# Kernel tuning notes

Hardware: AMD Instinct MI355X
Metric: run time of the kernel (lower is better)

Reference implementation:

```python
import jax, jax.numpy as jnp
import numpy as np

B, N, L = 16, 128, 512            # batch, scan length, per-step feature (= configs.seq_len)
D, S, K, R, H = 1024, 16, 4, 64, 2048  # d_model, d_state, ker_size, dt_rank, hidden_dimention


def _mamba_params(key, scale=0.02):
    ks = jax.random.split(key, 6)
    return dict(
        in_w=jax.random.normal(ks[0], (2 * D, L)) * scale,
        conv_w=jax.random.normal(ks[1], (D, K)) * scale,
        conv_b=jnp.zeros((D,)),
        xproj_w=jax.random.normal(ks[2], (R + 2 * S, D)) * scale,
        dt_w=jax.random.normal(ks[3], (D, R)) * scale,
        dt_b=jax.random.normal(ks[4], (D,)) * scale,
        A_log=jnp.tile(jnp.log(jnp.arange(1, S + 1, dtype=jnp.float32)), (D, 1)),
        Dp=jnp.ones((D,)),
        out_w=jax.random.normal(ks[5], (L, D)) * scale,
    )


def setup_inputs():
    key = jax.random.key(0)
    kx, kf, kr, k1, k2 = jax.random.split(key, 5)
    inp = {"x": jax.random.normal(kx, (B, N, L), dtype=jnp.float32)}
    for pre, k in (("f_", kf), ("r_", kr)):
        for n, v in _mamba_params(k).items():
            inp[pre + n] = v
    inp["pu_w"] = jax.random.normal(k1, (H, L)) * 0.02
    inp["pu_b"] = jnp.zeros((H,))
    inp["pl_w"] = jax.random.normal(k2, (L, H)) * 0.02
    inp["pl_b"] = jnp.zeros((L,))
    inp["ln_g"] = jnp.ones((L,))
    inp["ln_b"] = jnp.zeros((L,))
    return inp


def _ln(x, g, b, eps=1e-5):
    m = x.mean(-1, keepdims=True)
    v = ((x - m) ** 2).mean(-1, keepdims=True)
    return (x - m) * jax.lax.rsqrt(v + eps) * g + b


def _dw_causal_conv(x, w, b):
    # x: [B,N,D]; depthwise causal conv along N with kernel [D,K]
    xt = jnp.pad(x.transpose(0, 2, 1), ((0, 0), (0, 0), (K - 1, 0)))  # [B,D,N+K-1]
    y = jax.lax.conv_general_dilated(xt, w[:, None, :], (1,), 'VALID',
                                     dimension_numbers=('NCH', 'OIH', 'NCH'),
                                     feature_group_count=D)
    return (y + b[None, :, None]).transpose(0, 2, 1)


def _mamba(x, in_w, conv_w, conv_b, xproj_w, dt_w, dt_b, A_log, Dp, out_w):
    # standard Mamba block (in_proj -> depthwise conv -> silu -> selective scan -> gate -> out_proj)
    xi, res = jnp.split(x @ in_w.T, 2, axis=-1)             # [B,N,D] each
    xc = jax.nn.silu(_dw_causal_conv(xi, conv_w, conv_b))   # [B,N,D]
    dbc = xc @ xproj_w.T                                    # [B,N,R+2S]
    dt, Bm, Cm = dbc[..., :R], dbc[..., R:R + S], dbc[..., R + S:]
    delta = jax.nn.softplus(dt @ dt_w.T + dt_b)             # [B,N,D]
    A = -jnp.exp(A_log)                                     # [D,S]
    dA = jnp.exp(delta[..., None] * A)                      # [B,N,D,S]
    dBx = delta[..., None] * Bm[:, :, None, :] * xc[..., None]

    def step(h, t):
        dA_t, dBx_t, C_t = t
        h = dA_t * h + dBx_t                                # [B,D,S]
        return h, jnp.einsum('bds,bs->bd', h, C_t)

    _, ys = jax.lax.scan(step, jnp.zeros((x.shape[0], D, S), x.dtype),
                         (dA.transpose(1, 0, 2, 3), dBx.transpose(1, 0, 2, 3), Cm.transpose(1, 0, 2)))
    y = ys.transpose(1, 0, 2) + xc * Dp                     # [B,N,D]
    y = y * jax.nn.silu(res)
    return y @ out_w.T                                      # [B,N,L]


def reference(x, f_in_w, f_conv_w, f_conv_b, f_xproj_w, f_dt_w, f_dt_b, f_A_log, f_Dp, f_out_w,
              r_in_w, r_conv_w, r_conv_b, r_xproj_w, r_dt_w, r_dt_b, r_A_log, r_Dp, r_out_w,
              pu_w, pu_b, pl_w, pl_b, ln_g, ln_b):
    y1 = _mamba(x, f_in_w, f_conv_w, f_conv_b, f_xproj_w, f_dt_w, f_dt_b, f_A_log, f_Dp, f_out_w)
    y2 = _mamba(x[:, ::-1, :], r_in_w, r_conv_w, r_conv_b, r_xproj_w, r_dt_w, r_dt_b, r_A_log, r_Dp, r_out_w)
    y3 = _ln(x + y1 + y2[:, ::-1, :], ln_g, ln_b)
    yp = jax.nn.relu(y3 @ pu_w.T + pu_b)
    yp = yp @ pl_w.T + pl_b
    return _ln(yp + y3, ln_g, ln_b)
```

## Files before the change

### kernel.cpp

```cpp
#include <hip/hip_runtime.h>
#include <hip/hip_bf16.h>
#include <cstdint>

typedef __hip_bfloat16 bf16;

constexpr int Bb = 16, Nn = 128, Ll = 512, Dd = 1024, Ss = 16, Rr = 64, Hh = 2048;
constexpr int Mm = Bb * Nn;
#define LOG2E 1.44269504088896340736f

using bf16x8 = __attribute__((ext_vector_type(8))) __bf16;
using bf16x4 = __attribute__((ext_vector_type(4))) __bf16;
using f32x4  = __attribute__((ext_vector_type(4))) float;

__device__ __forceinline__ float to_f(float x) { return x; }
__device__ __forceinline__ float to_f(bf16 x) { return __bfloat162float(x); }
__device__ __forceinline__ void store_t(float* p, float v) { *p = v; }
__device__ __forceinline__ void store_t(bf16* p, float v) { *p = __float2bfloat16(v); }
__device__ __forceinline__ __bf16 cvt1(float x) {
  bf16 h = __float2bfloat16(x);
  return *reinterpret_cast<__bf16*>(&h);
}
__device__ __forceinline__ float bfraw_to_f(__bf16 x) {
  bf16 h = *reinterpret_cast<bf16*>(&x);
  return __bfloat162float(h);
}
__device__ __forceinline__ bf16x8 load8(const bf16* p) { return *(const bf16x8*)p; }
__device__ __forceinline__ bf16x8 load8(const float* p) {
  float4 a = *(const float4*)p;
  float4 b = *(const float4*)(p + 4);
  bf16x8 r;
  r[0] = cvt1(a.x); r[1] = cvt1(a.y); r[2] = cvt1(a.z); r[3] = cvt1(a.w);
  r[4] = cvt1(b.x); r[5] = cvt1(b.y); r[6] = cvt1(b.z); r[7] = cvt1(b.w);
  return r;
}
__device__ __forceinline__ bf16x8 load8rt(const void* p, size_t idx, int isbf) {
  if (isbf) return load8((const bf16*)p + idx);
  return load8((const float*)p + idx);
}
__device__ __forceinline__ float ldf(const void* p, int i, int isbf) {
  if (isbf) return __bfloat162float(((const bf16*)p)[i]);
  return ((const float*)p)[i];
}
__device__ __forceinline__ void gld16(const bf16* g, __bf16* l) {
  __builtin_amdgcn_global_load_lds(
      (const __attribute__((address_space(1))) void*)g,
      (__attribute__((address_space(3))) void*)l, 16, 0, 0);
}

enum { EPI_STORE = 0, EPI_BIAS_RELU = 1, EPI_ADD = 3, EPI_BIAS = 4, EPI_BIAS_SOFTPLUS = 5,
       EPI_ATOMIC = 6 };

__global__ void sniff_kernel(const unsigned short* __restrict__ xs, int* __restrict__ flags) {
  const int tid = threadIdx.x;
  int cnt = 0;
  for (int j = 0; j < 64; ++j) {
    int i = tid + j * 256;
    unsigned short u = xs[(size_t)i * 64];
    bf16 h = *reinterpret_cast<bf16*>(&u);
    float v = __bfloat162float(h);
    float a = fabsf(v);
    if (v == 0.f || (a > 0.0009765625f && a < 16.f)) ++cnt;
  }
  __shared__ int sc[256];
  sc[tid] = cnt;
  __syncthreads();
  for (int o = 128; o > 0; o >>= 1) {
    if (tid < o) sc[tid] += sc[tid + o];
    __syncthreads();
  }
  if (tid == 0) flags[0] = (sc[0] > 8192) ? 1 : 0;
}

__global__ __launch_bounds__(256) void prep_kernel(
    const int* __restrict__ flagp, const void* __restrict__ x,
    float* __restrict__ ZB, unsigned short* __restrict__ Xb,
    float* __restrict__ zerop,
    const void* __restrict__ fin, const void* __restrict__ rin,
    const void* __restrict__ fout, const void* __restrict__ rout,
    const void* __restrict__ puw, const void* __restrict__ plw,
    bf16* __restrict__ WBin, bf16* __restrict__ WBout,
    bf16* __restrict__ WBpu, bf16* __restrict__ WBpl) {
  const int isbf = *flagp;
  const int i = blockIdx.x * 256 + threadIdx.x;
  if (i < 262144) {
    float4 o;
    ushort4 u;
    if (isbf) {
      u = ((const ushort4*)x)[i];
      bf16 h0 = *reinterpret_cast<bf16*>(&u.x), h1 = *reinterpret_cast<bf16*>(&u.y);
      bf16 h2 = *reinterpret_cast<bf16*>(&u.z), h3 = *reinterpret_cast<bf16*>(&u.w);
      o = float4{__bfloat162float(h0), __bfloat162float(h1),
                 __bfloat162float(h2), __bfloat162float(h3)};
    } else {
      o = ((const float4*)x)[i];
      bf16 h0 = __float2bfloat16(o.x), h1 = __float2bfloat16(o.y);
      bf16 h2 = __float2bfloat16(o.z), h3 = __float2bfloat16(o.w);
      u = ushort4{*(unsigned short*)&h0, *(unsigned short*)&h1,
                  *(unsigned short*)&h2, *(unsigned short*)&h3};
    }
    ((float4*)ZB)[i] = o;
    ((ushort4*)Xb)[i] = u;
  } else if (i < 622592) {
    ((float4*)zerop)[i - 262144] = float4{0.f, 0.f, 0.f, 0.f};
  } else {
    const int j = i - 622592;
    const void* src;
    bf16* dst;
    int si;
    if (j < 131072) { src = fin; si = j; dst = WBin + (size_t)si * 8; }
    else if (j < 262144) { src = rin; si = j - 131072; dst = WBin + (size_t)1048576 + (size_t)si * 8; }
    else if (j < 393216) { src = puw; si = j - 262144; dst = WBpu + (size_t)si * 8; }
    else if (j < 524288) { src = plw; si = j - 393216; dst = WBpl + (size_t)si * 8; }
    else if (j < 589824) {
      src = fout; si = j - 524288;
      int e = si * 8;
      dst = WBout + (size_t)(e >> 10) * 2048 + (e & 1023);
    } else {
      src = rout; si = j - 589824;
      int e = si * 8;
      dst = WBout + (size_t)(e >> 10) * 2048 + 1024 + (e & 1023);
    }
    *(bf16x8*)dst = load8rt(src, (size_t)si * 8, isbf);
  }
}

constexpr int LDT2 = 72;

template <typename TC, int EPI>
__global__ __launch_bounds__(256) void gemm_rt(
    const int* __restrict__ flagp,
    const void* __restrict__ A, int lda, int abf,
    const void* __restrict__ Bw, const void* __restrict__ Bw2, int ldb,
    int bmode, int bsplit,
    TC* __restrict__ C, int ldc,
    const void* __restrict__ bias, const void* __restrict__ bias2,
    int N, int Kchunk, int zk, size_t a_doff, size_t c_doff) {
  const int isbf = *flagp;
  const int ab = (abf == 2) ? isbf : abf;
  __shared__ __align__(16) __bf16 As[64 * LDT2];
  __shared__ __align__(16) __bf16 Bs[64 * LDT2];
  const int tid = threadIdx.x;
  const int wave = tid >> 6, lane = tid & 63;
  const int quad = lane >> 4, l16 = lane & 15;
  const int wm = wave & 1, wn = wave >> 1;
  int bx = blockIdx.x, by = blockIdx.y;
  const int gx = gridDim.x, gy = gridDim.y;
  if ((gx & 7) == 0) {
    int id = bx + gx * by;
    int xcd = id & 7, sl = id >> 3;
    by = sl % gy;
    bx = (sl / gy) * 8 + xcd;
  }
  int zsl = blockIdx.z;
  const void* Ap = A;
  const void* Bp0 = Bw;
  const void* biasp = bias;
  if (bmode == 3) {
    const int dir = zsl / zk;
    zsl = zsl % zk;
    if (dir) {
      Ap = (const char*)A + a_doff * (size_t)(ab ? 2 : 4);
      C += c_doff;
      Bp0 = Bw2;
      biasp = bias2;
    }
  }
  const int m0 = by * 64, n0 = bx * 64;
  const int kb = zsl * Kchunk;
  const int srow = tid >> 3;
  const int scol = (tid & 7) * 8;
  f32x4 acc[2][2] = {};
  for (int k0 = kb; k0 < kb + Kchunk; k0 += 64) {
#pragma unroll
    for (int h = 0; h < 2; ++h) {
      int r = srow + h * 32;
      *(bf16x8*)(&As[r * LDT2 + scol]) =
          load8rt(Ap, (size_t)(m0 + r) * lda + k0 + scol, ab);
      int rb = n0 + r;
      rb = rb < N ? rb : N - 1;
      size_t bi = (size_t)rb * ldb + k0 + scol;
      *(bf16x8*)(&Bs[r * LDT2 + scol]) = load8rt(Bp0, bi, isbf);
    }
    __syncthreads();
#pragma unroll
    for (int kk2 = 0; kk2 < 2; ++kk2) {
      bf16x8 af[2], bfr[2];
#pragma unroll
      for (int i = 0; i < 2; ++i)
        af[i] = *(const bf16x8*)(&As[(wm * 32 + i * 16 + l16) * LDT2 + kk2 * 32 + quad * 8]);
#pragma unroll
      for (int j = 0; j < 2; ++j)
        bfr[j] = *(const bf16x8*)(&Bs[(wn * 32 + j * 16 + l16) * LDT2 + kk2 * 32 + quad * 8]);
#pragma unroll
      for (int i = 0; i < 2; ++i)
#pragma unroll
        for (int j = 0; j < 2; ++j)
          acc[i][j] = __builtin_amdgcn_mfma_f32_16x16x32_bf16(af[i], bfr[j], acc[i][j], 0, 0, 0);
    }
    __syncthreads();
  }
#pragma unroll
  for (int i = 0; i < 2; ++i) {
#pragma unroll
    for (int j = 0; j < 2; ++j) {
      const int col = n0 + wn * 32 + j * 16 + l16;
      if (col >= N) continue;
      float bv = 0.f;
      if (EPI == EPI_BIAS_RELU || EPI == EPI_BIAS || EPI == EPI_BIAS_SOFTPLUS)
        bv = ldf(biasp, col, isbf);
#pragma unroll
      for (int r = 0; r < 4; ++r) {
        const int row = m0 + wm * 32 + i * 16 + quad * 4 + r;
        size_t idx = (size_t)row * ldc + col;
        float v = acc[i][j][r];
        if (EPI == EPI_STORE) store_t(&C[idx], v);
        else if (EPI == EPI_BIAS_RELU) { v += bv; store_t(&C[idx], v > 0.f ? v : 0.f); }
        else if (EPI == EPI_BIAS) store_t(&C[idx], v + bv);
        else if (EPI == EPI_BIAS_SOFTPLUS) {
          v += bv;
          store_t(&C[idx], (v > 20.f) ? v : log1pf(__expf(v)));
        } else if (EPI == EPI_ATOMIC) {
          atomicAdd((float*)&C[idx], v);
        }
      }
    }
  }
}

template <typename TC, int EPI>
__global__ __launch_bounds__(256) void gemm128n(
    const int* __restrict__ flagp,
    const bf16* __restrict__ A, int lda,
    const bf16* __restrict__ Bw, int ldb,
    TC* __restrict__ C, int ldc,
    const void* __restrict__ bias,
    int Kchunk) {
  __shared__ __align__(16) __bf16 As[128 * 64];
  __shared__ __align__(16) __bf16 Bs[128 * 64];
  const int tid = threadIdx.x;
  const int wave = tid >> 6, lane = tid & 63;
  const int quad = lane >> 4, l16 = lane & 15;
  const int wr = wave >> 1, wc = wave & 1;
  int bx = blockIdx.x, by = blockIdx.y;
  const int gx = gridDim.x, gy = gridDim.y;
  if ((gx & 7) == 0) {
    int id = bx + gx * by;
    int xcd = id & 7, sl = id >> 3;
    by = sl % gy;
    bx = (sl / gy) * 8 + xcd;
  }
  const int m0 = by * 128, n0 = bx * 128;
  const int kb = blockIdx.z * Kchunk;
  const int lr = lane >> 3;
  const int lc = (lane & 7) * 8;
  f32x4 acc[4][4] = {};
  for (int k0 = kb; k0 < kb + Kchunk; k0 += 64) {
#pragma unroll
    for (int rr = 0; rr < 4; ++rr) {
      const int rowb = rr * 32 + wave * 8;
      gld16(A + (size_t)(m0 + rowb + lr) * lda + k0 + lc, &As[rowb * 64]);
      gld16(Bw + (size_t)(n0 + rowb + lr) * ldb + k0 + lc, &Bs[rowb * 64]);
    }
    __syncthreads();
#pragma unroll
    for (int kk = 0; kk < 2; ++kk) {
      bf16x8 af[4], bfr[4];
#pragma unroll
      for (int i = 0; i < 4; ++i)
        af[i] = *(const bf16x8*)(&As[(wr * 64 + i * 16 + l16) * 64 + kk * 32 + quad * 8]);
#pragma unroll
      for (int j = 0; j < 4; ++j)
        bfr[j] = *(const bf16x8*)(&Bs[(wc * 64 + j * 16 + l16) * 64 + kk * 32 + quad * 8]);
#pragma unroll
      for (int i = 0; i < 4; ++i)
#pragma unroll
        for (int j = 0; j < 4; ++j)
          acc[i][j] = __builtin_amdgcn_mfma_f32_16x16x32_bf16(af[i], bfr[j], acc[i][j], 0, 0, 0);
    }
    __syncthreads();
  }
  const int isbf = *flagp;
#pragma unroll
  for (int i = 0; i < 4; ++i) {
#pragma unroll
    for (int j = 0; j < 4; ++j) {
      const int col = n0 + wc * 64 + j * 16 + l16;
      float bv = 0.f;
      if (EPI == EPI_BIAS_RELU) bv = ldf(bias, col, isbf);
#pragma unroll
      for (int r = 0; r < 4; ++r) {
        const int row = m0 + wr * 64 + i * 16 + quad * 4 + r;
        size_t idx = (size_t)row * ldc + col;
        float v = acc[i][j][r];
        if (EPI == EPI_STORE) store_t(&C[idx], v);
        else if (EPI == EPI_BIAS_RELU) { v += bv; store_t(&C[idx], v > 0.f ? v : 0.f); }
        else if (EPI == EPI_ATOMIC) atomicAdd((float*)&C[idx], v);
      }
    }
  }
}

__global__ __launch_bounds__(256) void conv_silu_rt(
    const int* __restrict__ flagp, const bf16* __restrict__ X2b,
    const void* __restrict__ fcw, const void* __restrict__ fcb,
    const void* __restrict__ rcw, const void* __restrict__ rcb,
    bf16* __restrict__ XCb) {
  const int isbf = *flagp;
  const int dir = blockIdx.y >> 2;
  const int d = (blockIdx.y & 3) * 256 + threadIdx.x;
  const int m = blockIdx.x;
  const int t = m & (Nn - 1);
  const void* cw = dir ? rcw : fcw;
  const void* cb = dir ? rcb : fcb;
  float w0 = ldf(cw, d * 4 + 0, isbf), w1 = ldf(cw, d * 4 + 1, isbf);
  float w2 = ldf(cw, d * 4 + 2, isbf), w3 = ldf(cw, d * 4 + 3, isbf);
  float a = ldf(cb, d, isbf);
  const size_t base = (size_t)m * 4096 + (size_t)dir * 2048 + d;
  if (dir == 0) {
    if (t >= 3) a += w0 * to_f(X2b[base - 3 * 4096]);
    if (t >= 2) a += w1 * to_f(X2b[base - 2 * 4096]);
    if (t >= 1) a += w2 * to_f(X2b[base - 1 * 4096]);
    a += w3 * to_f(X2b[base]);
  } else {
    if (t + 3 < Nn) a += w0 * to_f(X2b[base + 3 * 4096]);
    if (t + 2 < Nn) a += w1 * to_f(X2b[base + 2 * 4096]);
    if (t + 1 < Nn) a += w2 * to_f(X2b[base + 1 * 4096]);
    a += w3 * to_f(X2b[base]);
  }
  const float s = a / (1.f + __builtin_amdgcn_exp2f(-a * LOG2E));
  XCb[(size_t)m * 2048 + (size_t)dir * 1024 + d] = __float2bfloat16(s);
}

__global__ __launch_bounds__(128) void scan_gate4(
    const int* __restrict__ flagp,
    const float* __restrict__ DBC0, bf16* __restrict__ XCb, const bf16* __restrict__ X2b,
    const bf16* __restrict__ DELTA0,
    const void* __restrict__ fAlog, const void* __restrict__ fDp,
    const void* __restrict__ rAlog, const void* __restrict__ rDp) {
  const int isbf = *flagp;
  const int dir = blockIdx.z;
  const float* DBC = DBC0 + (size_t)dir * Mm * 96;
  const bf16* DELTA = DELTA0 + (size_t)dir * Mm * 1024;
  const void* A_log = dir ? rAlog : fAlog;
  const void* Dp = dir ? rDp : fDp;
  __shared__ __align__(16) __bf16 sBC[Nn * 32];
  __shared__ __align__(16) __bf16 sD[Nn * 32];
  __shared__ __align__(16) __bf16 sX[Nn * 32];
  __shared__ __align__(16) __bf16 sG[Nn * 32];
  __shared__ __align__(16) __bf16 sY[Nn * 32];
  const int b = blockIdx.x;
  const int d0 = blockIdx.y * 32;
  const int tid = threadIdx.x;
  const size_t rowbase = (size_t)b * Nn;
  const size_t xc_col = (size_t)dir * 1024;
#pragma unroll
  for (int k = 0; k < 8; ++k) {
    int idx = tid + k * 128;
    int t = idx >> 3, c = idx & 7;
    float4 v = *(const float4*)(DBC + (rowbase + t) * 96 + 64 + c * 4);
    bf16x4 pv = {cvt1(v.x), cvt1(v.y), cvt1(v.z), cvt1(v.w)};
    int dst = (c < 4) ? (t * 32 + c * 8) : (t * 32 + (c - 4) * 8 + 4);
    *(bf16x4*)&sBC[dst] = pv;
  }
#pragma unroll
  for (int k = 0; k < 4; ++k) {
    int idx = tid + k * 128;
    int t = idx >> 2, h = idx & 3;
    *(uint4*)&sD[t * 32 + h * 8] =
        *(const uint4*)(DELTA + (rowbase + t) * 1024 + d0 + h * 8);
    *(uint4*)&sX[t * 32 + h * 8] =
        *(const uint4*)(XCb + (rowbase + t) * 2048 + xc_col + d0 + h * 8);
    bf16x8 rv = *(const bf16x8*)(X2b + (rowbase + t) * 4096 + (size_t)dir * 2048 + 1024 + d0 + h * 8);
    bf16x8 gv;
#pragma unroll
    for (int e = 0; e < 8; ++e) {
      float r = bfraw_to_f(rv[e]);
      gv[e] = cvt1(r / (1.f + __builtin_amdgcn_exp2f(-r * LOG2E)));
    }
    *(bf16x8*)&sG[t * 32 + h * 8] = gv;
  }
  __syncthreads();
  const int wv = tid >> 6, lane = tid & 63;
  const int dl = lane & 15, sg = lane >> 4;
  const int d_local = wv * 16 + dl;
  const int d = d0 + d_local;
  float A_[4];
#pragma unroll
  for (int j = 0; j < 4; ++j)
    A_[j] = -__expf(ldf(A_log, d * Ss + sg * 4 + j, isbf)) * LOG2E;
  const float dp = ldf(Dp, d, isbf);
  float h0 = 0.f, h1 = 0.f, h2 = 0.f, h3 = 0.f;
  for (int pg = 0; pg < Nn / 8; ++pg) {
    float accs[8], xvs[8];
#pragma unroll
    for (int u = 0; u < 8; ++u) {
      const int p = pg * 8 + u;
      const int t = dir ? (Nn - 1 - p) : p;
      const float dv = bfraw_to_f(sD[t * 32 + d_local]);
      const float xv = bfraw_to_f(sX[t * 32 + d_local]);
      bf16x8 bc = *(const bf16x8*)&sBC[t * 32 + sg * 8];
      const float dx = dv * xv;
      h0 = __builtin_amdgcn_exp2f(dv * A_[0]) * h0 + dx * bfraw_to_f(bc[0]);
      h1 = __builtin_amdgcn_exp2f(dv * A_[1]) * h1 + dx * bfraw_to_f(bc[1]);
      h2 = __builtin_amdgcn_exp2f(dv * A_[2]) * h2 + dx * bfraw_to_f(bc[2]);
      h3 = __builtin_amdgcn_exp2f(dv * A_[3]) * h3 + dx * bfraw_to_f(bc[3]);
      accs[u] = h0 * bfraw_to_f(bc[4]) + h1 * bfraw_to_f(bc[5]) +
                h2 * bfraw_to_f(bc[6]) + h3 * bfraw_to_f(bc[7]);
      xvs[u] = xv;
    }
#pragma unroll
    for (int u = 0; u < 8; ++u) {
      float a = accs[u];
      a += __shfl_xor(a, 16, 64);
      a += __shfl_xor(a, 32, 64);
      if (sg == 0) {
        const int p = pg * 8 + u;
        const int t = dir ? (Nn - 1 - p) : p;
        const float g = bfraw_to_f(sG[t * 32 + d_local]);
        sY[t * 32 + d_local] = cvt1((a + xvs[u] * dp) * g);
      }
    }
  }
  __syncthreads();
#pragma unroll
  for (int k = 0; k < 4; ++k) {
    int idx = tid + k * 128;
    int t = idx >> 2, h = idx & 3;
    *(uint4*)(XCb + (rowbase + t) * 2048 + xc_col + d0 + h * 8) =
        *(const uint4*)&sY[t * 32 + h * 8];
  }
}

template <int MODE>
__global__ __launch_bounds__(256) void ln_rt(const int* __restrict__ flagp,
                                             const float* __restrict__ Z,
                                             const float* __restrict__ Zadd,
                                             const void* __restrict__ g,
                                             const void* __restrict__ bb,
                                             const void* __restrict__ pb,
                                             void* __restrict__ outp,
                                             bf16* __restrict__ outp2) {
  const int isbf = *flagp;
  const int row = blockIdx.x;
  const int tid = threadIdx.x;
  const int c0 = tid * 2;
  const float2* z = (const float2*)(Z + (size_t)row * Ll);
  float2 v = z[tid];
  if (MODE == 1) {
    const float2* za = (const float2*)(Zadd + (size_t)row * Ll);
    float2 a = za[tid];
    v.x += a.x + ldf(pb, c0, isbf);
    v.y += a.y + ldf(pb, c0 + 1, isbf);
  }
  float s = v.x + v.y, q = v.x * v.x + v.y * v.y;
#pragma unroll
  for (int o = 32; o > 0; o >>= 1) {
    s += __shfl_xor(s, o, 64);
    q += __shfl_xor(q, o, 64);
  }
  __shared__ float ss[4], qq[4];
  const int wv = tid >> 6, ln = tid & 63;
  if (ln == 0) { ss[wv] = s; qq[wv] = q; }
  __syncthreads();
  s = ss[0] + ss[1] + ss[2] + ss[3];
  q = qq[0] + qq[1] + qq[2] + qq[3];
  const float mean = s * (1.f / Ll);
  const float var = q * (1.f / Ll) - mean * mean;
  const float rs = rsqrtf(var + 1e-5f);
  const float o0 = (v.x - mean) * rs * ldf(g, c0, isbf) + ldf(bb, c0, isbf);
  const float o1 = (v.y - mean) * rs * ldf(g, c0 + 1, isbf) + ldf(bb, c0 + 1, isbf);
  if (MODE == 0) {
    float* out = (float*)outp;
    out[(size_t)row * Ll + c0] = o0;
    out[(size_t)row * Ll + c0 + 1] = o1;
    outp2[(size_t)row * Ll + c0] = __float2bfloat16(o0);
    outp2[(size_t)row * Ll + c0 + 1] = __float2bfloat16(o1);
  } else {
    if (isbf) {
      bf16* out = (bf16*)outp;
      out[(size_t)row * Ll + c0] = __float2bfloat16(o0);
      out[(size_t)row * Ll + c0 + 1] = __float2bfloat16(o1);
    } else {
      float* out = (float*)outp;
      out[(size_t)row * Ll + c0] = o0;
      out[(size_t)row * Ll + c0 + 1] = o1;
    }
  }
}

extern "C" void kernel_launch(void* const* d_in, const int* in_sizes, int n_in, void* d_out,
                              int out_size, void* d_ws, size_t ws_size, hipStream_t stream) {
  char* ws = (char*)d_ws;
  int* flags = (int*)ws;
  bf16* X2b = (bf16*)(ws + 256);
  bf16* XCb = X2b + (size_t)Mm * 4096;
  bf16* Y3b = XCb + (size_t)Mm * 2048;
  bf16* DELTA = Y3b + (size_t)Mm * 512;
  bf16* Xb = DELTA + (size_t)2 * Mm * 1024;
  bf16* WBin = Xb + (size_t)Mm * 512;
  bf16* WBout = WBin + (size_t)4096 * 512;
  bf16* WBpu = WBout + (size_t)512 * 2048;
  bf16* WBpl = WBpu + (size_t)2048 * 512;
  float* DBC = (float*)(WBpl + (size_t)512 * 2048);
  float* Z2 = DBC + (size_t)2 * Mm * 96;
  float* ZB = Z2 + (size_t)Mm * 512;
  float* Y3 = ZB + (size_t)Mm * 512;
  bf16* H1 = X2b;
  size_t needed = 256 +
                  2 * ((size_t)Mm * 4096 + (size_t)Mm * 2048 + (size_t)Mm * 512 +
                       (size_t)2 * Mm * 1024 + (size_t)Mm * 512 +
                       (size_t)4096 * 512 + (size_t)512 * 2048 +
                       (size_t)2048 * 512 + (size_t)512 * 2048) +
                  4 * ((size_t)2 * Mm * 96 + (size_t)3 * Mm * 512);
  if (ws_size < needed) return;

  const void* x = d_in[0];
  const dim3 blk(256);

  sniff_kernel<<<dim3(1), blk, 0, stream>>>((const unsigned short*)x, flags);
  prep_kernel<<<dim3(4992), blk, 0, stream>>>(
      flags, x, ZB, (unsigned short*)Xb, DBC,
      d_in[1], d_in[10], d_in[9], d_in[18], d_in[19], d_in[21],
      WBin, WBout, WBpu, WBpl);
  gemm128n<bf16, EPI_STORE><<<dim3(32, 16), blk, 0, stream>>>(
      flags, Xb, Ll, WBin, Ll, X2b, 4096, nullptr, Ll);
  conv_silu_rt<<<dim3(Mm, 8), blk, 0, stream>>>(flags, X2b, d_in[2], d_in[3],
                                                d_in[11], d_in[12], XCb);
  gemm_rt<float, EPI_ATOMIC><<<dim3(2, 32, 8), blk, 0, stream>>>(
      flags, XCb, 2048, 1, d_in[4], d_in[13], Dd, 3, 0,
      DBC, 96, nullptr, nullptr, 96, 256, 4, 1024, (size_t)Mm * 96);
  gemm_rt<bf16, EPI_BIAS_SOFTPLUS><<<dim3(16, 32, 2), blk, 0, stream>>>(
      flags, DBC, 96, 0, d_in[5], d_in[14], Rr, 3, 0,
      DELTA, 1024, d_in[6], d_in[15], 1024, Rr, 1, (size_t)Mm * 96, (size_t)Mm * 1024);
  scan_gate4<<<dim3(Bb, Dd / 32, 2), dim3(128), 0, stream>>>(
      flags, DBC, XCb, X2b, DELTA, d_in[7], d_in[8], d_in[16], d_in[17]);
  gemm128n<float, EPI_ATOMIC><<<dim3(4, 16, 4), blk, 0, stream>>>(
      flags, XCb, 2048, WBout, 2048, ZB, Ll, nullptr, Ll);
  ln_rt<0><<<dim3(Mm), blk, 0, stream>>>(flags, ZB, nullptr, d_in[23], d_in[24], nullptr,
                                         (void*)Y3, Y3b);
  gemm128n<bf16, EPI_BIAS_RELU><<<dim3(16, 16), blk, 0, stream>>>(
      flags, Y3b, Ll, WBpu, Ll, H1, Hh, d_in[20], Ll);
  gemm128n<float, EPI_ATOMIC><<<dim3(4, 16, 4), blk, 0, stream>>>(
      flags, H1, Hh, WBpl, 2048, Z2, Ll, nullptr, Ll);
  ln_rt<1><<<dim3(Mm), blk, 0, stream>>>(flags, Z2, Y3, d_in[23], d_in[24], d_in[22],
                                         d_out, nullptr);

  (void)in_sizes; (void)n_in; (void)out_size;
}
```

Baseline: 336.7 us.

## Double-buffer gemm128n LDS tiles and write scan output directly to global

The 128x128 GEMM now keeps two LDS buffers, issuing loads for the next K tile before computing on the current one, so global loads can overlap MFMA work with one barrier per iteration. The scan kernel drops its shared output staging buffer and writes each gated result straight to global memory as scalar bf16 stores, with a smaller unroll of 4 steps. Doubling LDS (64KB per block) may cut GEMM occupancy, and the scattered 2-byte global stores in the scan may coalesce worse than the old 16-byte vector stores.

Result: no change. 336.5 us (-0.1%).

```diff
diff --git a/kernel.cpp b/kernel.cpp
--- a/kernel.cpp
+++ b/kernel.cpp
@@ -235,8 +235,8 @@
     TC* __restrict__ C, int ldc,
     const void* __restrict__ bias,
     int Kchunk) {
-  __shared__ __align__(16) __bf16 As[128 * 64];
-  __shared__ __align__(16) __bf16 Bs[128 * 64];
+  __shared__ __align__(16) __bf16 As[2][128 * 64];
+  __shared__ __align__(16) __bf16 Bs[2][128 * 64];
   const int tid = threadIdx.x;
   const int wave = tid >> 6, lane = tid & 63;
   const int quad = lane >> 4, l16 = lane & 15;
@@ -251,26 +251,32 @@
   }
   const int m0 = by * 128, n0 = bx * 128;
   const int kb = blockIdx.z * Kchunk;
+  const int kend = kb + Kchunk;
   const int lr = lane >> 3;
   const int lc = (lane & 7) * 8;
-  f32x4 acc[4][4] = {};
-  for (int k0 = kb; k0 < kb + Kchunk; k0 += 64) {
+  auto STAGE = [&](int buf, int k0) {
 #pragma unroll
     for (int rr = 0; rr < 4; ++rr) {
       const int rowb = rr * 32 + wave * 8;
-      gld16(A + (size_t)(m0 + rowb + lr) * lda + k0 + lc, &As[rowb * 64]);
-      gld16(Bw + (size_t)(n0 + rowb + lr) * ldb + k0 + lc, &Bs[rowb * 64]);
-    }
-    __syncthreads();
+      gld16(A + (size_t)(m0 + rowb + lr) * lda + k0 + lc, &As[buf][rowb * 64]);
+      gld16(Bw + (size_t)(n0 + rowb + lr) * ldb + k0 + lc, &Bs[buf][rowb * 64]);
+    }
+  };
+  f32x4 acc[4][4] = {};
+  int cur = 0;
+  STAGE(0, kb);
+  __syncthreads();
+  for (int k0 = kb; k0 < kend; k0 += 64) {
+    if (k0 + 64 < kend) STAGE(cur ^ 1, k0 + 64);
 #pragma unroll
     for (int kk = 0; kk < 2; ++kk) {
       bf16x8 af[4], bfr[4];
 #pragma unroll
       for (int i = 0; i < 4; ++i)
-        af[i] = *(const bf16x8*)(&As[(wr * 64 + i * 16 + l16) * 64 + kk * 32 + quad * 8]);
+        af[i] = *(const bf16x8*)(&As[cur][(wr * 64 + i * 16 + l16) * 64 + kk * 32 + quad * 8]);
 #pragma unroll
       for (int j = 0; j < 4; ++j)
-        bfr[j] = *(const bf16x8*)(&Bs[(wc * 64 + j * 16 + l16) * 64 + kk * 32 + quad * 8]);
+        bfr[j] = *(const bf16x8*)(&Bs[cur][(wc * 64 + j * 16 + l16) * 64 + kk * 32 + quad * 8]);
 #pragma unroll
       for (int i = 0; i < 4; ++i)
 #pragma unroll
@@ -278,6 +284,7 @@
           acc[i][j] = __builtin_amdgcn_mfma_f32_16x16x32_bf16(af[i], bfr[j], acc[i][j], 0, 0, 0);
     }
     __syncthreads();
+    cur ^= 1;
   }
   const int isbf = *flagp;
 #pragma unroll
@@ -331,7 +338,7 @@
   XCb[(size_t)m * 2048 + (size_t)dir * 1024 + d] = __float2bfloat16(s);
 }
 
-__global__ __launch_bounds__(128) void scan_gate4(
+__global__ __launch_bounds__(128) void scan_gate3(
     const int* __restrict__ flagp,
     const float* __restrict__ DBC0, bf16* __restrict__ XCb, const bf16* __restrict__ X2b,
     const bf16* __restrict__ DELTA0,
@@ -347,7 +354,6 @@
   __shared__ __align__(16) __bf16 sD[Nn * 32];
   __shared__ __align__(16) __bf16 sX[Nn * 32];
   __shared__ __align__(16) __bf16 sG[Nn * 32];
-  __shared__ __align__(16) __bf16 sY[Nn * 32];
   const int b = blockIdx.x;
   const int d0 = blockIdx.y * 32;
   const int tid = threadIdx.x;
@@ -390,11 +396,11 @@
     A_[j] = -__expf(ldf(A_log, d * Ss + sg * 4 + j, isbf)) * LOG2E;
   const float dp = ldf(Dp, d, isbf);
   float h0 = 0.f, h1 = 0.f, h2 = 0.f, h3 = 0.f;
-  for (int pg = 0; pg < Nn / 8; ++pg) {
-    float accs[8], xvs[8];
-#pragma unroll
-    for (int u = 0; u < 8; ++u) {
-      const int p = pg * 8 + u;
+  for (int pg = 0; pg < Nn / 4; ++pg) {
+    float accs[4], xvs[4];
+#pragma unroll
+    for (int u = 0; u < 4; ++u) {
+      const int p = pg * 4 + u;
       const int t = dir ? (Nn - 1 - p) : p;
       const float dv = bfraw_to_f(sD[t * 32 + d_local]);
       const float xv = bfraw_to_f(sX[t * 32 + d_local]);
@@ -409,25 +415,17 @@
       xvs[u] = xv;
     }
 #pragma unroll
-    for (int u = 0; u < 8; ++u) {
+    for (int u = 0; u < 4; ++u) {
       float a = accs[u];
       a += __shfl_xor(a, 16, 64);
       a += __shfl_xor(a, 32, 64);
       if (sg == 0) {
-        const int p = pg * 8 + u;
+        const int p = pg * 4 + u;
         const int t = dir ? (Nn - 1 - p) : p;
         const float g = bfraw_to_f(sG[t * 32 + d_local]);
-        sY[t * 32 + d_local] = cvt1((a + xvs[u] * dp) * g);
+        XCb[(rowbase + t) * 2048 + xc_col + d] = __float2bfloat16((a + xvs[u] * dp) * g);
       }
     }
-  }
-  __syncthreads();
-#pragma unroll
-  for (int k = 0; k < 4; ++k) {
-    int idx = tid + k * 128;
-    int t = idx >> 2, h = idx & 3;
-    *(uint4*)(XCb + (rowbase + t) * 2048 + xc_col + d0 + h * 8) =
-        *(const uint4*)&sY[t * 32 + h * 8];
   }
 }
 
@@ -532,7 +530,7 @@
   gemm_rt<bf16, EPI_BIAS_SOFTPLUS><<<dim3(16, 32, 2), blk, 0, stream>>>(
       flags, DBC, 96, 0, d_in[5], d_in[14], Rr, 3, 0,
       DELTA, 1024, d_in[6], d_in[15], 1024, Rr, 1, (size_t)Mm * 96, (size_t)Mm * 1024);
-  scan_gate4<<<dim3(Bb, Dd / 32, 2), dim3(128), 0, stream>>>(
+  scan_gate3<<<dim3(Bb, Dd / 32, 2), dim3(128), 0, stream>>>(
       flags, DBC, XCb, X2b, DELTA, d_in[7], d_in[8], d_in[16], d_in[17]);
   gemm128n<float, EPI_ATOMIC><<<dim3(4, 16, 4), blk, 0, stream>>>(
       flags, XCb, 2048, WBout, 2048, ZB, Ll, nullptr, Ll);
```
